# Performance work log

Hardware: AMD Instinct MI355X
Metric: run time of the kernel (lower is better)

Reference implementation:

```python
import jax, jax.numpy as jnp
import numpy as np

EMBED_DIM = 256
NUM_EMB = 4096
LIMIT = 0.01


def setup_inputs() -> dict:
    key = jax.random.key(0)
    k1, k2 = jax.random.split(key)
    x = jax.random.normal(k1, (32, 32, 32, EMBED_DIM), dtype=jnp.float32)
    # codebook initialized uniform(-limit, limit), stored as [D, K] like the torch module
    vectors = jax.random.uniform(k2, (EMBED_DIM, NUM_EMB), dtype=jnp.float32,
                                 minval=-LIMIT, maxval=LIMIT)
    return {"x": x, "vectors": vectors}


def reference(x, vectors):
    B = x.shape[0]
    flat_x = x.reshape(-1, EMBED_DIM)                       # [N, D]
    distances = (jnp.sum(flat_x * flat_x, axis=1, keepdims=True)
                 - 2.0 * flat_x @ vectors
                 + jnp.sum(vectors * vectors, axis=0, keepdims=True))
    encoding_indices = jnp.argmin(distances, axis=1)        # [N]
    quantized_flat = vectors.T[encoding_indices]            # gather rows of [K, D]
    quantized_x = quantized_flat.reshape(x.shape)
    dictionary_loss = jnp.mean((jax.lax.stop_gradient(x) - quantized_x) ** 2)
    commitment_loss = jnp.mean((x - jax.lax.stop_gradient(quantized_x)) ** 2)
    # straight-through estimator
    quantized_x = x + jax.lax.stop_gradient(quantized_x - x)
    return (quantized_x, dictionary_loss, commitment_loss,
            encoding_indices.reshape(B, -1))
```

## Files before the change

### kernel.cpp

```cpp
#include <hip/hip_runtime.h>
#include <math.h>

#define D_DIM 256
#define K_NUM 4096
#define N_ROWS 32768
#define QCAP 3072
#define MARGIN 0.02f

typedef _Float16 half8 __attribute__((ext_vector_type(8)));
typedef float floatx4 __attribute__((ext_vector_type(4)));

__global__ __launch_bounds__(256) void vq_vv(const float* __restrict__ V,
                                             float* __restrict__ vv) {
  int k = blockIdx.x * 256 + threadIdx.x;
  float acc = 0.0f;
  for (int d = 0; d < D_DIM; ++d) {
    float v = V[(size_t)d * K_NUM + k];
    acc = __fadd_rn(acc, __fmul_rn(v, v));
  }
  vv[k] = acc;
}

__global__ __launch_bounds__(256) void vq_prep(const float* __restrict__ V,
                                               _Float16* __restrict__ vtb,
                                               float* __restrict__ vt,
                                               int write_vt) {
  __shared__ float tile[64][64];
  const int col0 = (blockIdx.x & 63) * 64;
  const int d0 = (blockIdx.x >> 6) * 64;
  const int cq = threadIdx.x >> 6;
  const int cl = threadIdx.x & 63;
#pragma unroll
  for (int it = 0; it < 16; ++it) {
    int d = it * 4 + cq;
    tile[d][cl] = V[(size_t)(d0 + d) * K_NUM + col0 + cl];
  }
  __syncthreads();
#pragma unroll
  for (int qq = 0; qq < 2; ++qq) {
    int q = cq * 2 + qq;
    half8 h;
#pragma unroll
    for (int j = 0; j < 8; ++j) h[j] = (_Float16)tile[q * 8 + j][cl];
    *(half8*)(vtb + ((size_t)(d0 / 8 + q) * K_NUM + col0 + cl) * 8) = h;
  }
  if (write_vt) {
#pragma unroll
    for (int j = 0; j < 4; ++j) {
      int d = cq * 16 + j * 4;
      float4 f;
      f.x = tile[d + 0][cl]; f.y = tile[d + 1][cl];
      f.z = tile[d + 2][cl]; f.w = tile[d + 3][cl];
      *(float4*)(vt + (size_t)(col0 + cl) * D_DIM + d0 + d) = f;
    }
  }
}

struct alignas(16) ScreenShared {
  _Float16 a[64 * 256];
  float vvs[K_NUM];
  float xxs[64];
  float wmin[8][64];
  float thr[64];
  unsigned long long best[64];
  unsigned qbuf[QCAP];
  int qn;
};

__device__ __forceinline__ void vq_push(ScreenShared& sh, int r, int col) {
  int u = atomicAdd(&sh.qn, 1);
  if (u < QCAP) sh.qbuf[u] = ((unsigned)r << 12) | (unsigned)col;
}

template <int MODE>
__device__ __forceinline__ void vq_cell(ScreenShared& sh,
                                        const _Float16* __restrict__ vtb,
                                        float* tb, int w, int l, int c) {
  const int g = l >> 4, ln = l & 15;
  const int cb = w * 512 + c * 32;
  const float vv0 = sh.vvs[cb + ln];
  const float vv1 = sh.vvs[cb + 16 + ln];

  const int abase = (ln << 8) ^ ((g ^ (ln & 7)) << 3);
  const char* bp = (const char*)vtb + (((size_t)g * K_NUM + cb + ln) << 4);

  floatx4 acc[4][2];
#pragma unroll
  for (int rf = 0; rf < 4; ++rf)
#pragma unroll
    for (int cf = 0; cf < 2; ++cf) acc[rf][cf] = {0.f, 0.f, 0.f, 0.f};

  half8 afb[2][4], bfb[2][2];
  bfb[0][0] = *(const half8*)bp;
  bfb[0][1] = *(const half8*)(bp + 256);
#pragma unroll
  for (int rf = 0; rf < 4; ++rf)
    afb[0][rf] = *(const half8*)(sh.a + abase + rf * 4096);

#pragma unroll
  for (int ks = 0; ks < 8; ++ks) {
    const int cur = ks & 1, nxt = cur ^ 1;
    if (ks < 7) {
      const int koff = (ks + 1) * 262144;
      bfb[nxt][0] = *(const half8*)(bp + koff);
      bfb[nxt][1] = *(const half8*)(bp + koff + 256);
      const int aoff = abase ^ ((ks + 1) << 5);
#pragma unroll
      for (int rf = 0; rf < 4; ++rf)
        afb[nxt][rf] = *(const half8*)(sh.a + aoff + rf * 4096);
    }
#pragma unroll
    for (int rf = 0; rf < 4; ++rf)
#pragma unroll
      for (int cf = 0; cf < 2; ++cf)
        acc[rf][cf] = __builtin_amdgcn_mfma_f32_16x16x32_f16(
            afb[cur][rf], bfb[cur][cf], acc[rf][cf], 0, 0, 0);
  }

#pragma unroll
  for (int rf = 0; rf < 4; ++rf) {
#pragma unroll
    for (int reg = 0; reg < 4; ++reg) {
      float s0v = fmaf(-2.0f, acc[rf][0][reg], vv0);
      float s1v = fmaf(-2.0f, acc[rf][1][reg], vv1);
      float m = fminf(s0v, s1v);
      if (MODE == 0) {
        tb[rf * 4 + reg] = fminf(tb[rf * 4 + reg], m);
      } else {
        float thr = tb[rf * 4 + reg];
        if (m <= thr) {
          const int r = rf * 16 + g * 4 + reg;
          if (s0v <= thr) vq_push(sh, r, cb + ln);
          if (s1v <= thr) vq_push(sh, r, cb + 16 + ln);
        }
      }
    }
  }
}

__global__ __launch_bounds__(512, 4) void vq_screen(
    const float* __restrict__ X, const float* __restrict__ V,
    const _Float16* __restrict__ vtb, const float* __restrict__ vvp,
    const float* __restrict__ vt, float* __restrict__ idx_out,
    float* __restrict__ outq, float* __restrict__ loss_sum) {
  __shared__ ScreenShared sh;
  const int tid = threadIdx.x;
  const int w = tid >> 6, l = tid & 63;
  const int row0 = blockIdx.x * 64;

#pragma unroll
  for (int it = 0; it < 4; ++it) {
    int idx = it * 512 + tid;
    int r = idx >> 5, s = idx & 31;
    const float* xp = X + (size_t)(row0 + r) * D_DIM + s * 8;
    float4 v0 = *(const float4*)xp, v1 = *(const float4*)(xp + 4);
    half8 h;
    h[0] = (_Float16)v0.x; h[1] = (_Float16)v0.y;
    h[2] = (_Float16)v0.z; h[3] = (_Float16)v0.w;
    h[4] = (_Float16)v1.x; h[5] = (_Float16)v1.y;
    h[6] = (_Float16)v1.z; h[7] = (_Float16)v1.w;
    int slot = (r << 5) | (s ^ (r & 7));
    *(half8*)&sh.a[slot * 8] = h;
  }
#pragma unroll
  for (int it = 0; it < 8; ++it) sh.vvs[it * 512 + tid] = vvp[it * 512 + tid];

  {
    const int grp = tid >> 4;
    const int half = (l >> 3) & 1, j = l & 7;
#pragma unroll
    for (int rr = 0; rr < 2; ++rr) {
      const int r = grp * 2 + rr;
      const float* p = X + (size_t)(row0 + r) * D_DIM + half * 128 + j;
      float v = p[0];
      float acc = __fmul_rn(v, v);
#pragma unroll
      for (int i = 1; i < 16; ++i) {
        v = p[i * 8];
        acc = __fadd_rn(acc, __fmul_rn(v, v));
      }
      acc = __fadd_rn(acc, __shfl_xor(acc, 1));
      acc = __fadd_rn(acc, __shfl_xor(acc, 2));
      acc = __fadd_rn(acc, __shfl_xor(acc, 4));
      acc = __fadd_rn(acc, __shfl_xor(acc, 8));
      if ((l & 15) == 0) sh.xxs[r] = acc;
    }
  }
  if (tid < 64) sh.best[tid] = 0xFFFFFFFFFFFFFFFFull;
  if (tid == 0) sh.qn = 0;
  __syncthreads();

  float tb[16];
#pragma unroll
  for (int i = 0; i < 16; ++i) tb[i] = INFINITY;

  vq_cell<0>(sh, vtb, tb, w, l, 0);
  vq_cell<0>(sh, vtb, tb, w, l, 8);

#pragma unroll
  for (int i = 0; i < 16; ++i) {
#pragma unroll
    for (int off = 1; off <= 8; off <<= 1)
      tb[i] = fminf(tb[i], __shfl_xor(tb[i], off));
  }
  {
    const int g = l >> 4, ln = l & 15;
    if (ln == 0) {
#pragma unroll
      for (int rf = 0; rf < 4; ++rf)
#pragma unroll
        for (int reg = 0; reg < 4; ++reg)
          sh.wmin[w][rf * 16 + g * 4 + reg] = tb[rf * 4 + reg];
    }
  }
  __syncthreads();
  if (tid < 64) {
    float m = sh.wmin[0][tid];
#pragma unroll
    for (int j = 1; j < 8; ++j) m = fminf(m, sh.wmin[j][tid]);
    sh.thr[tid] = m + MARGIN;
  }
  __syncthreads();
  {
    const int g = l >> 4;
#pragma unroll
    for (int rf = 0; rf < 4; ++rf)
#pragma unroll
      for (int reg = 0; reg < 4; ++reg)
        tb[rf * 4 + reg] = sh.thr[rf * 16 + g * 4 + reg];
  }

  for (int c = 0; c < 16; ++c) vq_cell<1>(sh, vtb, tb, w, l, c);
  __syncthreads();

  const int nq = min(sh.qn, QCAP);
  for (int i = w; i < nq; i += 8) {
    unsigned e = sh.qbuf[i];
    int r = (int)(e >> 12), col = (int)(e & 4095);
    float4 xv = *(const float4*)(X + (size_t)(row0 + r) * D_DIM + l * 4);
    float p = 0.f;
    if (vt) {
      float4 qv = *(const float4*)(vt + (size_t)col * D_DIM + l * 4);
      p = fmaf(xv.x, qv.x, p);
      p = fmaf(xv.y, qv.y, p);
      p = fmaf(xv.z, qv.z, p);
      p = fmaf(xv.w, qv.w, p);
    } else {
      const float* vp = V + col;
      p = fmaf(xv.x, vp[(size_t)(l * 4 + 0) * K_NUM], p);
      p = fmaf(xv.y, vp[(size_t)(l * 4 + 1) * K_NUM], p);
      p = fmaf(xv.z, vp[(size_t)(l * 4 + 2) * K_NUM], p);
      p = fmaf(xv.w, vp[(size_t)(l * 4 + 3) * K_NUM], p);
    }
#pragma unroll
    for (int off = 1; off < 64; off <<= 1) p += __shfl_xor(p, off);
    if (l == 0) {
      float s = __fadd_rn(__fsub_rn(sh.xxs[r], __fmul_rn(2.0f, p)),
                          sh.vvs[col]);
      unsigned long long key =
          ((unsigned long long)__float_as_uint(s) << 32) | (unsigned)col;
      atomicMin(&sh.best[r], key);
    }
  }
  __syncthreads();

  if (tid < 64)
    idx_out[row0 + tid] = (float)(unsigned)(sh.best[tid] & 0xFFFFFFFFu);

  float lsum = 0.f;
#pragma unroll
  for (int it = 0; it < 8; ++it) {
    int t = it * 512 + tid;
    int rloc = t >> 6;
    int c4 = (t & 63) << 2;
    int bi = (int)(unsigned)(sh.best[rloc] & 0xFFFFFFFFu);
    float4 xv = *(const float4*)(X + (size_t)(row0 + rloc) * D_DIM + c4);
    float4 qv;
    if (vt) {
      qv = *(const float4*)(vt + (size_t)bi * D_DIM + c4);
    } else {
      qv.x = V[(size_t)(c4 + 0) * K_NUM + bi];
      qv.y = V[(size_t)(c4 + 1) * K_NUM + bi];
      qv.z = V[(size_t)(c4 + 2) * K_NUM + bi];
      qv.w = V[(size_t)(c4 + 3) * K_NUM + bi];
    }
    float4 o;
    o.x = __fadd_rn(xv.x, __fsub_rn(qv.x, xv.x));
    o.y = __fadd_rn(xv.y, __fsub_rn(qv.y, xv.y));
    o.z = __fadd_rn(xv.z, __fsub_rn(qv.z, xv.z));
    o.w = __fadd_rn(xv.w, __fsub_rn(qv.w, xv.w));
    *(float4*)(outq + (size_t)(row0 + rloc) * D_DIM + c4) = o;
    float d0 = __fsub_rn(xv.x, qv.x), d1 = __fsub_rn(xv.y, qv.y);
    float d2 = __fsub_rn(xv.z, qv.z), d3 = __fsub_rn(xv.w, qv.w);
    lsum += d0 * d0 + d1 * d1 + d2 * d2 + d3 * d3;
  }
#pragma unroll
  for (int off = 1; off < 64; off <<= 1) lsum += __shfl_xor(lsum, off);
  __syncthreads();
  float* red = (float*)sh.qbuf;
  if (l == 0) red[w] = lsum;
  __syncthreads();
  if (tid == 0) {
    float s = red[0];
#pragma unroll
    for (int j = 1; j < 8; ++j) s += red[j];
    atomicAdd(loss_sum, s);
  }
}

__global__ void vq_fin(const float* __restrict__ loss_sum,
                       float* __restrict__ out_losses) {
  float m = loss_sum[0] / 8388608.0f;
  out_losses[0] = m;
  out_losses[1] = m;
}

extern "C" void kernel_launch(void* const* d_in, const int* in_sizes, int n_in,
                              void* d_out, int out_size, void* d_ws, size_t ws_size,
                              hipStream_t stream) {
  const float* x = (const float*)d_in[0];
  const float* V = (const float*)d_in[1];
  float* out = (float*)d_out;
  float* outq    = out;
  float* outloss = out + 8388608;
  float* outidx  = out + 8388610;

  float* ws_vv  = (float*)d_ws;
  float* ws_sum = ws_vv + K_NUM;
  _Float16* ws_vtb = (_Float16*)((char*)d_ws + 163840);
  float* ws_vt = (float*)((char*)d_ws + 163840 + 2097152);
  const int have_vt = (ws_size >= (size_t)(163840 + 2097152 + 4194304));
  float* vt_arg = have_vt ? ws_vt : (float*)nullptr;

  hipMemsetAsync(ws_sum, 0, sizeof(float), stream);
  vq_vv    <<<K_NUM / 256, 256, 0, stream>>>(V, ws_vv);
  vq_prep  <<<256, 256, 0, stream>>>(V, ws_vtb, ws_vt, have_vt);
  vq_screen<<<N_ROWS / 64, 512, 0, stream>>>(x, V, ws_vtb, ws_vv, vt_arg,
                                             outidx, outq, ws_sum);
  vq_fin   <<<1, 1, 0, stream>>>(ws_sum, outloss);
}
```

Baseline: 196.7 us.

## Hold X tile in registers, halve rows per block, drop LDS A buffer

The screening kernel now handles 32 rows per block instead of 64. The fp16 X fragments now live in registers for the whole kernel rather than being staged through a swizzled LDS tile, which removes the LDS A buffer and its per-k-step loads. MFMA sections are wrapped with s_setprio, output stores become nontemporal, and the launch bound drops from 4 to 2 blocks per CU. The trade-off is twice as many blocks, so codebook fragments are re-read from global/L2 twice as often per row, with higher register pressure. QCAP is reduced, which raises the risk of candidate-buffer overflow.

Measured after the change: 284.9 us. 44.8% more time.

```diff
diff --git a/kernel.cpp b/kernel.cpp
--- a/kernel.cpp
+++ b/kernel.cpp
@@ -4,7 +4,7 @@
 #define D_DIM 256
 #define K_NUM 4096
 #define N_ROWS 32768
-#define QCAP 3072
+#define QCAP 2048
 #define MARGIN 0.02f
 
 typedef _Float16 half8 __attribute__((ext_vector_type(8)));
@@ -57,12 +57,11 @@
 }
 
 struct alignas(16) ScreenShared {
-  _Float16 a[64 * 256];
   float vvs[K_NUM];
-  float xxs[64];
-  float wmin[8][64];
-  float thr[64];
-  unsigned long long best[64];
+  float xxs[32];
+  float wmin[8][32];
+  float thr[32];
+  unsigned long long best[32];
   unsigned qbuf[QCAP];
   int qn;
 };
@@ -75,50 +74,43 @@
 template <int MODE>
 __device__ __forceinline__ void vq_cell(ScreenShared& sh,
                                         const _Float16* __restrict__ vtb,
+                                        const half8 (&areg)[2][8],
                                         float* tb, int w, int l, int c) {
   const int g = l >> 4, ln = l & 15;
   const int cb = w * 512 + c * 32;
   const float vv0 = sh.vvs[cb + ln];
   const float vv1 = sh.vvs[cb + 16 + ln];
-
-  const int abase = (ln << 8) ^ ((g ^ (ln & 7)) << 3);
   const char* bp = (const char*)vtb + (((size_t)g * K_NUM + cb + ln) << 4);
 
-  floatx4 acc[4][2];
-#pragma unroll
-  for (int rf = 0; rf < 4; ++rf)
+  floatx4 acc[2][2];
+#pragma unroll
+  for (int rf = 0; rf < 2; ++rf)
 #pragma unroll
     for (int cf = 0; cf < 2; ++cf) acc[rf][cf] = {0.f, 0.f, 0.f, 0.f};
 
-  half8 afb[2][4], bfb[2][2];
+  half8 bfb[2][2];
   bfb[0][0] = *(const half8*)bp;
   bfb[0][1] = *(const half8*)(bp + 256);
-#pragma unroll
-  for (int rf = 0; rf < 4; ++rf)
-    afb[0][rf] = *(const half8*)(sh.a + abase + rf * 4096);
 
 #pragma unroll
   for (int ks = 0; ks < 8; ++ks) {
-    const int cur = ks & 1, nxt = cur ^ 1;
     if (ks < 7) {
       const int koff = (ks + 1) * 262144;
-      bfb[nxt][0] = *(const half8*)(bp + koff);
-      bfb[nxt][1] = *(const half8*)(bp + koff + 256);
-      const int aoff = abase ^ ((ks + 1) << 5);
-#pragma unroll
-      for (int rf = 0; rf < 4; ++rf)
-        afb[nxt][rf] = *(const half8*)(sh.a + aoff + rf * 4096);
-    }
-#pragma unroll
-    for (int rf = 0; rf < 4; ++rf)
+      bfb[(ks + 1) & 1][0] = *(const half8*)(bp + koff);
+      bfb[(ks + 1) & 1][1] = *(const half8*)(bp + koff + 256);
+    }
+    __builtin_amdgcn_s_setprio(1);
+#pragma unroll
+    for (int rf = 0; rf < 2; ++rf)
 #pragma unroll
       for (int cf = 0; cf < 2; ++cf)
         acc[rf][cf] = __builtin_amdgcn_mfma_f32_16x16x32_f16(
-            afb[cur][rf], bfb[cur][cf], acc[rf][cf], 0, 0, 0);
-  }
-
-#pragma unroll
-  for (int rf = 0; rf < 4; ++rf) {
+            areg[rf][ks], bfb[ks & 1][cf], acc[rf][cf], 0, 0, 0);
+    __builtin_amdgcn_s_setprio(0);
+  }
+
+#pragma unroll
+  for (int rf = 0; rf < 2; ++rf) {
 #pragma unroll
     for (int reg = 0; reg < 4; ++reg) {
       float s0v = fmaf(-2.0f, acc[rf][0][reg], vv0);
@@ -138,7 +130,7 @@
   }
 }
 
-__global__ __launch_bounds__(512, 4) void vq_screen(
+__global__ __launch_bounds__(512, 2) void vq_screen(
     const float* __restrict__ X, const float* __restrict__ V,
     const _Float16* __restrict__ vtb, const float* __restrict__ vvp,
     const float* __restrict__ vt, float* __restrict__ idx_out,
@@ -146,91 +138,85 @@
   __shared__ ScreenShared sh;
   const int tid = threadIdx.x;
   const int w = tid >> 6, l = tid & 63;
-  const int row0 = blockIdx.x * 64;
-
-#pragma unroll
-  for (int it = 0; it < 4; ++it) {
-    int idx = it * 512 + tid;
-    int r = idx >> 5, s = idx & 31;
-    const float* xp = X + (size_t)(row0 + r) * D_DIM + s * 8;
-    float4 v0 = *(const float4*)xp, v1 = *(const float4*)(xp + 4);
-    half8 h;
-    h[0] = (_Float16)v0.x; h[1] = (_Float16)v0.y;
-    h[2] = (_Float16)v0.z; h[3] = (_Float16)v0.w;
-    h[4] = (_Float16)v1.x; h[5] = (_Float16)v1.y;
-    h[6] = (_Float16)v1.z; h[7] = (_Float16)v1.w;
-    int slot = (r << 5) | (s ^ (r & 7));
-    *(half8*)&sh.a[slot * 8] = h;
-  }
+  const int g = l >> 4, ln = l & 15;
+  const int row0 = blockIdx.x * 32;
+
+  half8 areg[2][8];
+#pragma unroll
+  for (int rf = 0; rf < 2; ++rf) {
+#pragma unroll
+    for (int ks = 0; ks < 8; ++ks) {
+      const float* xp =
+          X + (size_t)(row0 + rf * 16 + ln) * D_DIM + (ks * 4 + g) * 8;
+      float4 v0 = *(const float4*)xp, v1 = *(const float4*)(xp + 4);
+      half8 h;
+      h[0] = (_Float16)v0.x; h[1] = (_Float16)v0.y;
+      h[2] = (_Float16)v0.z; h[3] = (_Float16)v0.w;
+      h[4] = (_Float16)v1.x; h[5] = (_Float16)v1.y;
+      h[6] = (_Float16)v1.z; h[7] = (_Float16)v1.w;
+      areg[rf][ks] = h;
+    }
+  }
+
 #pragma unroll
   for (int it = 0; it < 8; ++it) sh.vvs[it * 512 + tid] = vvp[it * 512 + tid];
 
   {
-    const int grp = tid >> 4;
-    const int half = (l >> 3) & 1, j = l & 7;
-#pragma unroll
-    for (int rr = 0; rr < 2; ++rr) {
-      const int r = grp * 2 + rr;
-      const float* p = X + (size_t)(row0 + r) * D_DIM + half * 128 + j;
-      float v = p[0];
-      float acc = __fmul_rn(v, v);
-#pragma unroll
-      for (int i = 1; i < 16; ++i) {
-        v = p[i * 8];
-        acc = __fadd_rn(acc, __fmul_rn(v, v));
-      }
-      acc = __fadd_rn(acc, __shfl_xor(acc, 1));
-      acc = __fadd_rn(acc, __shfl_xor(acc, 2));
-      acc = __fadd_rn(acc, __shfl_xor(acc, 4));
-      acc = __fadd_rn(acc, __shfl_xor(acc, 8));
-      if ((l & 15) == 0) sh.xxs[r] = acc;
-    }
-  }
-  if (tid < 64) sh.best[tid] = 0xFFFFFFFFFFFFFFFFull;
+    const int r = tid >> 4;
+    const int hv = (l >> 3) & 1, j = l & 7;
+    const float* p = X + (size_t)(row0 + r) * D_DIM + hv * 128 + j;
+    float v = p[0];
+    float acc = __fmul_rn(v, v);
+#pragma unroll
+    for (int i = 1; i < 16; ++i) {
+      v = p[i * 8];
+      acc = __fadd_rn(acc, __fmul_rn(v, v));
+    }
+    acc = __fadd_rn(acc, __shfl_xor(acc, 1));
+    acc = __fadd_rn(acc, __shfl_xor(acc, 2));
+    acc = __fadd_rn(acc, __shfl_xor(acc, 4));
+    acc = __fadd_rn(acc, __shfl_xor(acc, 8));
+    if ((l & 15) == 0) sh.xxs[r] = acc;
+  }
+  if (tid < 32) sh.best[tid] = 0xFFFFFFFFFFFFFFFFull;
   if (tid == 0) sh.qn = 0;
   __syncthreads();
 
-  float tb[16];
-#pragma unroll
-  for (int i = 0; i < 16; ++i) tb[i] = INFINITY;
-
-  vq_cell<0>(sh, vtb, tb, w, l, 0);
-  vq_cell<0>(sh, vtb, tb, w, l, 8);
-
-#pragma unroll
-  for (int i = 0; i < 16; ++i) {
+  float tb[8];
+#pragma unroll
+  for (int i = 0; i < 8; ++i) tb[i] = INFINITY;
+
+  vq_cell<0>(sh, vtb, areg, tb, w, l, 0);
+  vq_cell<0>(sh, vtb, areg, tb, w, l, 8);
+
+#pragma unroll
+  for (int i = 0; i < 8; ++i) {
 #pragma unroll
     for (int off = 1; off <= 8; off <<= 1)
       tb[i] = fminf(tb[i], __shfl_xor(tb[i], off));
   }
-  {
-    const int g = l >> 4, ln = l & 15;
-    if (ln == 0) {
-#pragma unroll
-      for (int rf = 0; rf < 4; ++rf)
-#pragma unroll
-        for (int reg = 0; reg < 4; ++reg)
-          sh.wmin[w][rf * 16 + g * 4 + reg] = tb[rf * 4 + reg];
-    }
-  }
-  __syncthreads();
-  if (tid < 64) {
+  if (ln == 0) {
+#pragma unroll
+    for (int rf = 0; rf < 2; ++rf)
+#pragma unroll
+      for (int reg = 0; reg < 4; ++reg)
+        sh.wmin[w][rf * 16 + g * 4 + reg] = tb[rf * 4 + reg];
+  }
+  __syncthreads();
+  if (tid < 32) {
     float m = sh.wmin[0][tid];
 #pragma unroll
     for (int j = 1; j < 8; ++j) m = fminf(m, sh.wmin[j][tid]);
     sh.thr[tid] = m + MARGIN;
   }
   __syncthreads();
-  {
-    const int g = l >> 4;
-#pragma unroll
-    for (int rf = 0; rf < 4; ++rf)
-#pragma unroll
-      for (int reg = 0; reg < 4; ++reg)
-        tb[rf * 4 + reg] = sh.thr[rf * 16 + g * 4 + reg];
-  }
-
-  for (int c = 0; c < 16; ++c) vq_cell<1>(sh, vtb, tb, w, l, c);
+#pragma unroll
+  for (int rf = 0; rf < 2; ++rf)
+#pragma unroll
+    for (int reg = 0; reg < 4; ++reg)
+      tb[rf * 4 + reg] = sh.thr[rf * 16 + g * 4 + reg];
+
+  for (int c = 0; c < 16; ++c) vq_cell<1>(sh, vtb, areg, tb, w, l, c);
   __syncthreads();
 
   const int nq = min(sh.qn, QCAP);
@@ -264,12 +250,12 @@
   }
   __syncthreads();
 
-  if (tid < 64)
+  if (tid < 32)
     idx_out[row0 + tid] = (float)(unsigned)(sh.best[tid] & 0xFFFFFFFFu);
 
   float lsum = 0.f;
 #pragma unroll
-  for (int it = 0; it < 8; ++it) {
+  for (int it = 0; it < 4; ++it) {
     int t = it * 512 + tid;
     int rloc = t >> 6;
     int c4 = (t & 63) << 2;
@@ -284,12 +270,13 @@
       qv.z = V[(size_t)(c4 + 2) * K_NUM + bi];
       qv.w = V[(size_t)(c4 + 3) * K_NUM + bi];
     }
-    float4 o;
-    o.x = __fadd_rn(xv.x, __fsub_rn(qv.x, xv.x));
-    o.y = __fadd_rn(xv.y, __fsub_rn(qv.y, xv.y));
-    o.z = __fadd_rn(xv.z, __fsub_rn(qv.z, xv.z));
-    o.w = __fadd_rn(xv.w, __fsub_rn(qv.w, xv.w));
-    *(float4*)(outq + (size_t)(row0 + rloc) * D_DIM + c4) = o;
+    floatx4 o;
+    o[0] = __fadd_rn(xv.x, __fsub_rn(qv.x, xv.x));
+    o[1] = __fadd_rn(xv.y, __fsub_rn(qv.y, xv.y));
+    o[2] = __fadd_rn(xv.z, __fsub_rn(qv.z, xv.z));
+    o[3] = __fadd_rn(xv.w, __fsub_rn(qv.w, xv.w));
+    __builtin_nontemporal_store(
+        o, (floatx4*)(outq + (size_t)(row0 + rloc) * D_DIM + c4));
     float d0 = __fsub_rn(xv.x, qv.x), d1 = __fsub_rn(xv.y, qv.y);
     float d2 = __fsub_rn(xv.z, qv.z), d3 = __fsub_rn(xv.w, qv.w);
     lsum += d0 * d0 + d1 * d1 + d2 * d2 + d3 * d3;
@@ -335,7 +322,7 @@
   hipMemsetAsync(ws_sum, 0, sizeof(float), stream);
   vq_vv    <<<K_NUM / 256, 256, 0, stream>>>(V, ws_vv);
   vq_prep  <<<256, 256, 0, stream>>>(V, ws_vtb, ws_vt, have_vt);
-  vq_screen<<<N_ROWS / 64, 512, 0, stream>>>(x, V, ws_vtb, ws_vv, vt_arg,
+  vq_screen<<<N_ROWS / 32, 512, 0, stream>>>(x, V, ws_vtb, ws_vv, vt_arg,
                                              outidx, outq, ws_sum);
   vq_fin   <<<1, 1, 0, stream>>>(ws_sum, outloss);
 }
```
